# Kernel tuning notes

Hardware: AMD Instinct MI355X
Metric: run time of the kernel (lower is better)

The kernel has to match this reference:

```python
import jax, jax.numpy as jnp
import numpy as np

N = 50000   # nodes
E = 800000  # edges
NF = 16     # num_node_features
EF = 8      # num_edge_features
H = 4       # heads
C = 64      # out_channels per head
NC = 4      # num_classes


def setup_inputs() -> dict:
    key = jax.random.key(0)
    ks = jax.random.split(key, 32)
    w = lambda k, shape: (jax.random.normal(k, shape, jnp.float32) * 0.05)
    inp = {
        "x": jax.random.normal(ks[0], (N, NF), jnp.float32),
        "edge_index": jax.random.randint(ks[1], (2, E), 0, N, dtype=jnp.int32),
        "edge_attr": jax.random.normal(ks[2], (E, EF), jnp.float32),
        # fc00
        "w00": w(ks[3], (NF, 64)), "b00": jnp.zeros((64,), jnp.float32),
        # edge MLP
        "we1": w(ks[4], (EF, 64)), "be1": jnp.zeros((64,), jnp.float32),
        "we2": w(ks[5], (64, 64)), "be2": jnp.zeros((64,), jnp.float32),
        "we3": w(ks[6], (64, 64)), "be3": jnp.zeros((64,), jnp.float32),
        # TransformerConv projections (64 -> H*C = 256)
        "wq": w(ks[7], (64, H * C)), "bq": jnp.zeros((H * C,), jnp.float32),
        "wk": w(ks[8], (64, H * C)), "bk": jnp.zeros((H * C,), jnp.float32),
        "wv": w(ks[9], (64, H * C)), "bv": jnp.zeros((H * C,), jnp.float32),
        "wedge": w(ks[10], (64, H * C)), "bedge": jnp.zeros((H * C,), jnp.float32),
        "wskip": w(ks[11], (64, H * C)), "bskip": jnp.zeros((H * C,), jnp.float32),
        # LayerNorm(256)
        "ln_g": jnp.ones((H * C,), jnp.float32), "ln_b": jnp.zeros((H * C,), jnp.float32),
        # head
        "w1": w(ks[12], (H * C, 128)), "b1": jnp.zeros((128,), jnp.float32),
        "w2": w(ks[13], (128, NC)), "b2": jnp.zeros((NC,), jnp.float32),
    }
    return inp


def _forward(x, edge_attr, w00, b00, we1, be1, we2, be2, we3, be3,
             wq, bq, wk, bk, wv, bv, wedge, bedge, wskip, bskip,
             ln_g, ln_b, w1, b1, w2, b2, edge_index):
    relu = jax.nn.relu
    n = x.shape[0]
    # node embed (dropout = identity in eval)
    x1 = relu(x @ w00 + b00)                              # [N, 64]
    # edge MLP
    e = relu(edge_attr @ we1 + be1)
    e = relu(e @ we2 + be2)
    e = relu(e @ we3 + be3)                               # [E, 64]
    src, dst = edge_index[0], edge_index[1]
    # project nodes once, then gather per edge
    q = (x1 @ wq + bq).reshape(n, H, C)[dst]              # [E, H, C]
    k = (x1 @ wk + bk).reshape(n, H, C)[src]
    v = (x1 @ wv + bv).reshape(n, H, C)[src]
    eh = (e @ wedge + bedge).reshape(-1, H, C)            # [E, H, C]
    k = k + eh
    v = v + eh
    alpha = jnp.sum(q * k, axis=-1) / np.sqrt(C)          # [E, H]
    # segment softmax over incoming edges of each target node
    m = jax.ops.segment_max(alpha, dst, num_segments=n)   # [N, H]
    m = jnp.where(jnp.isfinite(m), m, 0.0)
    p = jnp.exp(alpha - m[dst])
    s = jax.ops.segment_sum(p, dst, num_segments=n)
    a = p / (s[dst] + 1e-16)                              # [E, H]
    out = jax.ops.segment_sum(v * a[:, :, None], dst, num_segments=n)
    out = out.reshape(n, H * C) + (x1 @ wskip + bskip)    # root skip (root_weight=True)
    # LayerNorm(256)
    mu = jnp.mean(out, axis=-1, keepdims=True)
    var = jnp.mean(jnp.square(out - mu), axis=-1, keepdims=True)
    out = (out - mu) * jax.lax.rsqrt(var + 1e-5) * ln_g + ln_b
    out = relu(out)
    h = relu(out @ w1 + b1)
    logits = h @ w2 + b2
    return jax.nn.log_softmax(logits, axis=1)


def reference(x, edge_index, edge_attr, w00, b00, we1, be1, we2, be2, we3, be3,
              wq, bq, wk, bk, wv, bv, wedge, bedge, wskip, bskip,
              ln_g, ln_b, w1, b1, w2, b2):
    return _forward(x, edge_attr, w00, b00, we1, be1, we2, be2, we3, be3,
                    wq, bq, wk, bk, wv, bv, wedge, bedge, wskip, bskip,
                    ln_g, ln_b, w1, b1, w2, b2, edge_index)
```

## Files before the change

### kernel.cpp

```cpp
#include <hip/hip_runtime.h>
#include <hip/hip_bf16.h>

typedef unsigned short u16;
typedef __attribute__((ext_vector_type(8))) short bf16x8;
typedef __attribute__((ext_vector_type(4))) float f32x4;

#define NN 50000
#define NE 800000
#define SCAN_NB ((NN + 255) / 256)

__device__ __forceinline__ float bf2f(u16 u) { return __uint_as_float(((unsigned)u) << 16); }
__device__ __forceinline__ u16 f2bf(float f) {
  unsigned u = __float_as_uint(f);
  return (u16)((u + 0x7FFFu + ((u >> 16) & 1u)) >> 16);
}

__global__ void k_zero(int* __restrict__ deg) {
  int i = blockIdx.x * 256 + threadIdx.x;
  if (i < NN) deg[i] = 0;
}

__global__ void k_hist(const int* __restrict__ ei, int* __restrict__ deg) {
  int i = blockIdx.x * 256 + threadIdx.x;
  if (i < NE) {
    int d = ei[NE + i];
    if (d >= 0 && d < NN) atomicAdd(&deg[d], 1);
  }
}

__global__ __launch_bounds__(256) void k_scan_a(const int* __restrict__ deg,
                                                int* __restrict__ bsum) {
  __shared__ int red[256];
  const int t = threadIdx.x;
  const int i = blockIdx.x * 256 + t;
  red[t] = (i < NN) ? deg[i] : 0;
  __syncthreads();
  #pragma unroll
  for (int s = 128; s > 0; s >>= 1) {
    if (t < s) red[t] += red[t + s];
    __syncthreads();
  }
  if (t == 0) bsum[blockIdx.x] = red[0];
}

__global__ __launch_bounds__(256) void k_scan_b(const int* __restrict__ bsum,
                                                int* __restrict__ boff,
                                                int* __restrict__ rowptr) {
  __shared__ int s[256];
  const int t = threadIdx.x;
  int v = (t < SCAN_NB) ? bsum[t] : 0;
  s[t] = v;
  __syncthreads();
  #pragma unroll
  for (int o = 1; o < 256; o <<= 1) {
    int u = (t >= o) ? s[t - o] : 0;
    __syncthreads();
    s[t] += u;
    __syncthreads();
  }
  if (t < SCAN_NB) boff[t] = s[t] - v;
  if (t == 255) rowptr[NN] = s[255];
}

__global__ __launch_bounds__(256) void k_scan_c(const int* __restrict__ deg,
                                                const int* __restrict__ boff,
                                                int* __restrict__ rowptr,
                                                int* __restrict__ cursor) {
  __shared__ int s[256];
  const int t = threadIdx.x;
  const int i = blockIdx.x * 256 + t;
  int v = (i < NN) ? deg[i] : 0;
  s[t] = v;
  __syncthreads();
  #pragma unroll
  for (int o = 1; o < 256; o <<= 1) {
    int u = (t >= o) ? s[t - o] : 0;
    __syncthreads();
    s[t] += u;
    __syncthreads();
  }
  if (i < NN) {
    int r = boff[blockIdx.x] + s[t] - v;
    rowptr[i] = r;
    cursor[i] = r;
  }
}

__global__ void k_scatter(const int* __restrict__ ei, int* __restrict__ cursor,
                          int* __restrict__ slist, int* __restrict__ e2p) {
  int i = blockIdx.x * 256 + threadIdx.x;
  if (i < NE) {
    int d = ei[NE + i];
    if (d >= 0 && d < NN) {
      int pos = atomicAdd(&cursor[d], 1);
      if (pos >= 0 && pos < NE) {
        e2p[i] = pos;
        int s = ei[i];
        slist[pos] = max(0, min(s, NN - 1));
      }
    }
  }
}

__global__ void k_prep(const float* __restrict__ wedge, const float* __restrict__ wk,
                       float* __restrict__ wT, float* __restrict__ wkT) {
  int i = blockIdx.x * 256 + threadIdx.x;
  if (i < 16384) {
    int c = i >> 6, j = i & 63;
    wT[i] = wedge[j * 256 + c];
  } else if (i < 32768) {
    int i2 = i - 16384;
    int c = i2 >> 6, j = i2 & 63;
    wkT[i2] = wk[j * 256 + c];
  }
}

__global__ void k_prep_w(const float* __restrict__ we1, const float* __restrict__ we2,
                         const float* __restrict__ we3,
                         u16* __restrict__ wB1t, u16* __restrict__ wB2t, u16* __restrict__ wB3t) {
  int i = blockIdx.x * 256 + threadIdx.x;
  if (i < 512) {
    int n = i >> 3, k = i & 7;
    wB1t[i] = f2bf(we1[k * 64 + n]);
  } else if (i < 512 + 4096) {
    int i2 = i - 512;
    int n = i2 >> 6, k = i2 & 63;
    wB2t[i2] = f2bf(we2[k * 64 + n]);
  } else if (i < 512 + 8192) {
    int i2 = i - 512 - 4096;
    int n = i2 >> 6, k = i2 & 63;
    wB3t[i2] = f2bf(we3[k * 64 + n]);
  }
}

__global__ void k_prep_b(const float* __restrict__ wedge, const float* __restrict__ wv,
                         const float* __restrict__ wskip, u16* __restrict__ Bt) {
  const int col = blockIdx.x;
  const int k = threadIdx.x;
  float v;
  if (k < 256) v = ((k >> 6) == (col >> 6)) ? wedge[(k & 63) * 256 + col] : 0.f;
  else if (k < 512) { int k2 = k - 256; v = ((k2 >> 6) == (col >> 6)) ? wv[(k2 & 63) * 256 + col] : 0.f; }
  else v = wskip[(k - 512) * 256 + col];
  Bt[col * 576 + k] = f2bf(v);
}

__global__ void k_prep_h(const float* __restrict__ w1, u16* __restrict__ Bt1) {
  const int col = blockIdx.x;
  const int k = threadIdx.x;
  Bt1[col * 256 + k] = f2bf(w1[k * 128 + col]);
}

__global__ __launch_bounds__(256) void k_ng(
    const float* __restrict__ x, const float* __restrict__ w00, const float* __restrict__ b00,
    const float* __restrict__ wq, const float* __restrict__ bq,
    const float* __restrict__ wT, const float* __restrict__ wkT,
    u16* __restrict__ x1g, u16* __restrict__ Gg, u16* __restrict__ Qkg) {
  __shared__ float xs[128];
  __shared__ float x1s[8 * 65];
  __shared__ float qs[8 * 256];
  const int t = threadIdx.x;
  const int n0 = blockIdx.x * 8;
  if (t < 128) xs[t] = x[n0 * 16 + t];
  __syncthreads();
  #pragma unroll
  for (int it = 0; it < 2; ++it) {
    int nb = it * 4 + (t >> 6);
    int col = t & 63;
    float v = b00[col];
    #pragma unroll
    for (int i = 0; i < 16; ++i) v += xs[nb * 16 + i] * w00[i * 64 + col];
    v = fmaxf(v, 0.f);
    x1s[nb * 65 + col] = v;
    x1g[(n0 + nb) * 64 + col] = f2bf(v);
  }
  __syncthreads();
  {
    float aq[8];
    const float bqv = bq[t];
    #pragma unroll
    for (int nb = 0; nb < 8; ++nb) aq[nb] = bqv;
    for (int j = 0; j < 64; ++j) {
      float wqv = wq[j * 256 + t];
      #pragma unroll
      for (int nb = 0; nb < 8; ++nb) aq[nb] += x1s[nb * 65 + j] * wqv;
    }
    #pragma unroll
    for (int nb = 0; nb < 8; ++nb) qs[nb * 256 + t] = aq[nb];
  }
  __syncthreads();
  const int h = t >> 6, j = t & 63;
  float accG[8] = {0, 0, 0, 0, 0, 0, 0, 0};
  float accK[8] = {0, 0, 0, 0, 0, 0, 0, 0};
  for (int c = 0; c < 64; ++c) {
    float wv = wT[(h * 64 + c) * 64 + j];
    float wk = wkT[(h * 64 + c) * 64 + j];
    #pragma unroll
    for (int nb = 0; nb < 8; ++nb) {
      float qv = qs[nb * 256 + h * 64 + c];
      accG[nb] += qv * wv;
      accK[nb] += qv * wk;
    }
  }
  #pragma unroll
  for (int nb = 0; nb < 8; ++nb) {
    Gg[(n0 + nb) * 256 + t] = f2bf(accG[nb]);
    Qkg[(n0 + nb) * 256 + t] = f2bf(accK[nb]);
  }
}

#define EPB 128
#define APAD 72
__global__ __launch_bounds__(256) void k_edge_mlp(
    const float* __restrict__ ea,
    const u16* __restrict__ wB1t, const u16* __restrict__ wB2t, const u16* __restrict__ wB3t,
    const float* __restrict__ be1, const float* __restrict__ be2, const float* __restrict__ be3,
    const int* __restrict__ e2p, u16* __restrict__ e3g) {
  __shared__ u16 actA[EPB * APAD];
  __shared__ u16 actB[EPB * APAD];
  const int t = threadIdx.x;
  const int w = t >> 6, l = t & 63;
  const int quad = l >> 4, li = l & 15;
  const int e0 = blockIdx.x * EPB;
  const f32x4 zc = {0.f, 0.f, 0.f, 0.f};

  float b1c[4], b2c[4], b3c[4];
  #pragma unroll
  for (int nt = 0; nt < 4; ++nt) {
    b1c[nt] = be1[nt * 16 + li];
    b2c[nt] = be2[nt * 16 + li];
    b3c[nt] = be3[nt * 16 + li];
  }

  bf16x8 b1f[4];
  #pragma unroll
  for (int nt = 0; nt < 4; ++nt) {
    bf16x8 z = {};
    if (quad == 0) z = *(const bf16x8*)(wB1t + (nt * 16 + li) * 8);
    b1f[nt] = z;
  }
  #pragma unroll
  for (int mi = 0; mi < 2; ++mi) {
    const int mt = w * 2 + mi;
    bf16x8 af = {};
    if (quad == 0) {
      const float4* pa = (const float4*)(ea + (size_t)(e0 + mt * 16 + li) * 8);
      float4 p0 = pa[0], p1 = pa[1];
      af[0] = (short)f2bf(p0.x); af[1] = (short)f2bf(p0.y);
      af[2] = (short)f2bf(p0.z); af[3] = (short)f2bf(p0.w);
      af[4] = (short)f2bf(p1.x); af[5] = (short)f2bf(p1.y);
      af[6] = (short)f2bf(p1.z); af[7] = (short)f2bf(p1.w);
    }
    #pragma unroll
    for (int nt = 0; nt < 4; ++nt) {
      f32x4 d = __builtin_amdgcn_mfma_f32_16x16x32_bf16(af, b1f[nt], zc, 0, 0, 0);
      #pragma unroll
      for (int r = 0; r < 4; ++r)
        actA[(mt * 16 + quad * 4 + r) * APAD + nt * 16 + li] = f2bf(fmaxf(d[r] + b1c[nt], 0.f));
    }
  }
  __syncthreads();

  {
    bf16x8 bf[4][2];
    #pragma unroll
    for (int nt = 0; nt < 4; ++nt)
      #pragma unroll
      for (int kk = 0; kk < 2; ++kk)
        bf[nt][kk] = *(const bf16x8*)(wB2t + (nt * 16 + li) * 64 + kk * 32 + quad * 8);
    #pragma unroll
    for (int mi = 0; mi < 2; ++mi) {
      const int mt = w * 2 + mi;
      bf16x8 a0 = *(const bf16x8*)(actA + (mt * 16 + li) * APAD + quad * 8);
      bf16x8 a1 = *(const bf16x8*)(actA + (mt * 16 + li) * APAD + 32 + quad * 8);
      #pragma unroll
      for (int nt = 0; nt < 4; ++nt) {
        f32x4 d = __builtin_amdgcn_mfma_f32_16x16x32_bf16(a0, bf[nt][0], zc, 0, 0, 0);
        d = __builtin_amdgcn_mfma_f32_16x16x32_bf16(a1, bf[nt][1], d, 0, 0, 0);
        #pragma unroll
        for (int r = 0; r < 4; ++r)
          actB[(mt * 16 + quad * 4 + r) * APAD + nt * 16 + li] = f2bf(fmaxf(d[r] + b2c[nt], 0.f));
      }
    }
  }
  __syncthreads();

  {
    bf16x8 bf[4][2];
    #pragma unroll
    for (int nt = 0; nt < 4; ++nt)
      #pragma unroll
      for (int kk = 0; kk < 2; ++kk)
        bf[nt][kk] = *(const bf16x8*)(wB3t + (nt * 16 + li) * 64 + kk * 32 + quad * 8);
    #pragma unroll
    for (int mi = 0; mi < 2; ++mi) {
      const int mt = w * 2 + mi;
      bf16x8 a0 = *(const bf16x8*)(actB + (mt * 16 + li) * APAD + quad * 8);
      bf16x8 a1 = *(const bf16x8*)(actB + (mt * 16 + li) * APAD + 32 + quad * 8);
      #pragma unroll
      for (int nt = 0; nt < 4; ++nt) {
        f32x4 d = __builtin_amdgcn_mfma_f32_16x16x32_bf16(a0, bf[nt][0], zc, 0, 0, 0);
        d = __builtin_amdgcn_mfma_f32_16x16x32_bf16(a1, bf[nt][1], d, 0, 0, 0);
        #pragma unroll
        for (int r = 0; r < 4; ++r)
          actA[(mt * 16 + quad * 4 + r) * APAD + nt * 16 + li] = f2bf(fmaxf(d[r] + b3c[nt], 0.f));
      }
    }
  }
  __syncthreads();

  #pragma unroll
  for (int it = 0; it < 4; ++it) {
    int flat = it * 2048 + t * 8;
    int el = flat >> 6, c = flat & 63;
    int pos = e2p[e0 + el];
    pos = ((unsigned)pos <= (unsigned)(NE - 1)) ? pos : NE;
    uint4 v = *(const uint4*)(actA + el * APAD + c);
    *(uint4*)(e3g + (size_t)pos * 64 + c) = v;
  }
}

__global__ __launch_bounds__(256) void k_attn(
    const int* __restrict__ rowptr, const int* __restrict__ slist,
    u16* yo, const u16* __restrict__ x1g, u16* gz, const u16* __restrict__ Qkg,
    const u16* __restrict__ e3g, float* __restrict__ bfac) {
  const int t = threadIdx.x;
  const int w = t >> 6;
  const int l = t & 63;
  const int grp = l >> 4;
  const int li = l & 15;
  const int chb = grp * 64 + li * 4;
  const int n = blockIdx.x * 4 + w;
  int base = rowptr[n];
  int end  = rowptr[n + 1];
  base = max(0, min(base, NE));
  end  = max(base, min(end, NE));
  if (l == 0) bfac[n] = (end > base) ? 1.f : 0.f;

  float Qkf[4], Gf[4];
  {
    ushort4 kv = *(const ushort4*)(Qkg + (size_t)n * 256 + chb);
    Qkf[0] = bf2f(kv.x); Qkf[1] = bf2f(kv.y); Qkf[2] = bf2f(kv.z); Qkf[3] = bf2f(kv.w);
    ushort4 gv = *(const ushort4*)(gz + (size_t)n * 256 + chb);
    Gf[0] = bf2f(gv.x); Gf[1] = bf2f(gv.y); Gf[2] = bf2f(gv.z); Gf[3] = bf2f(gv.w);
  }

  float s_run = 0.f;
  float y[4] = {0, 0, 0, 0}, zz[4] = {0, 0, 0, 0};
  int d = base;
  for (; d + 1 < end; d += 2) {
    int src0 = slist[d], src1 = slist[d + 1];
    src0 = max(0, min(src0, NN - 1)); src1 = max(0, min(src1, NN - 1));
    ushort4 x0 = *(const ushort4*)(x1g + (size_t)src0 * 64 + li * 4);
    ushort4 e0 = *(const ushort4*)(e3g + (size_t)d * 64 + li * 4);
    ushort4 x1v = *(const ushort4*)(x1g + (size_t)src1 * 64 + li * 4);
    ushort4 e1 = *(const ushort4*)(e3g + (size_t)(d + 1) * 64 + li * 4);
    float xf00 = bf2f(x0.x), xf01 = bf2f(x0.y), xf02 = bf2f(x0.z), xf03 = bf2f(x0.w);
    float ef00 = bf2f(e0.x), ef01 = bf2f(e0.y), ef02 = bf2f(e0.z), ef03 = bf2f(e0.w);
    float xf10 = bf2f(x1v.x), xf11 = bf2f(x1v.y), xf12 = bf2f(x1v.z), xf13 = bf2f(x1v.w);
    float ef10 = bf2f(e1.x), ef11 = bf2f(e1.y), ef12 = bf2f(e1.z), ef13 = bf2f(e1.w);
    float p0 = Qkf[0]*xf00 + Qkf[1]*xf01 + Qkf[2]*xf02 + Qkf[3]*xf03
             + Gf[0]*ef00 + Gf[1]*ef01 + Gf[2]*ef02 + Gf[3]*ef03;
    float p1 = Qkf[0]*xf10 + Qkf[1]*xf11 + Qkf[2]*xf12 + Qkf[3]*xf13
             + Gf[0]*ef10 + Gf[1]*ef11 + Gf[2]*ef12 + Gf[3]*ef13;
    #pragma unroll
    for (int mk = 1; mk < 16; mk <<= 1) { p0 += __shfl_xor(p0, mk); p1 += __shfl_xor(p1, mk); }
    float w0 = __expf(fminf(p0 * 0.125f, 60.f));
    float w1 = __expf(fminf(p1 * 0.125f, 60.f));
    s_run += w0 + w1;
    y[0] += w0*xf00 + w1*xf10; y[1] += w0*xf01 + w1*xf11;
    y[2] += w0*xf02 + w1*xf12; y[3] += w0*xf03 + w1*xf13;
    zz[0] += w0*ef00 + w1*ef10; zz[1] += w0*ef01 + w1*ef11;
    zz[2] += w0*ef02 + w1*ef12; zz[3] += w0*ef03 + w1*ef13;
  }
  if (d < end) {
    int src0 = slist[d];
    src0 = max(0, min(src0, NN - 1));
    ushort4 x0 = *(const ushort4*)(x1g + (size_t)src0 * 64 + li * 4);
    ushort4 e0 = *(const ushort4*)(e3g + (size_t)d * 64 + li * 4);
    float xf00 = bf2f(x0.x), xf01 = bf2f(x0.y), xf02 = bf2f(x0.z), xf03 = bf2f(x0.w);
    float ef00 = bf2f(e0.x), ef01 = bf2f(e0.y), ef02 = bf2f(e0.z), ef03 = bf2f(e0.w);
    float p0 = Qkf[0]*xf00 + Qkf[1]*xf01 + Qkf[2]*xf02 + Qkf[3]*xf03
             + Gf[0]*ef00 + Gf[1]*ef01 + Gf[2]*ef02 + Gf[3]*ef03;
    #pragma unroll
    for (int mk = 1; mk < 16; mk <<= 1) p0 += __shfl_xor(p0, mk);
    float w0 = __expf(fminf(p0 * 0.125f, 60.f));
    s_run += w0;
    y[0] += w0*xf00; y[1] += w0*xf01; y[2] += w0*xf02; y[3] += w0*xf03;
    zz[0] += w0*ef00; zz[1] += w0*ef01; zz[2] += w0*ef02; zz[3] += w0*ef03;
  }
  const float inv_s = 1.0f / (s_run + 1e-16f);
  ushort4 ynv, znv;
  ynv.x = f2bf(y[0] * inv_s); ynv.y = f2bf(y[1] * inv_s);
  ynv.z = f2bf(y[2] * inv_s); ynv.w = f2bf(y[3] * inv_s);
  znv.x = f2bf(zz[0] * inv_s); znv.y = f2bf(zz[1] * inv_s);
  znv.z = f2bf(zz[2] * inv_s); znv.w = f2bf(zz[3] * inv_s);
  *(ushort4*)(yo + (size_t)n * 256 + chb) = ynv;
  *(ushort4*)(gz + (size_t)n * 256 + chb) = znv;
}

#define PM 64
#define PK 576
#define PAPAD 584
__global__ __launch_bounds__(256) void k_post(
    const u16* __restrict__ zng, const u16* __restrict__ yng, const u16* __restrict__ x1g,
    const u16* __restrict__ Bt, const float* __restrict__ bfac,
    const float* __restrict__ bedge, const float* __restrict__ bv, const float* __restrict__ bskip,
    const float* __restrict__ lng, const float* __restrict__ lnb,
    u16* __restrict__ postg) {
  __shared__ u16 As[PM * PAPAD];
  __shared__ float ps1[PM * 4];
  __shared__ float ps2[PM * 4];
  const int t = threadIdx.x;
  const int w = t >> 6, l = t & 63;
  const int quad = l >> 4, li = l & 15;
  const int n0 = blockIdx.x * PM;

  for (int q = t; q < 2048; q += 256) {
    int row = q >> 5, off = (q & 31) * 8;
    uint4 vz = make_uint4(0, 0, 0, 0), vy = make_uint4(0, 0, 0, 0);
    if (n0 + row < NN) {
      vz = *(const uint4*)(zng + (size_t)(n0 + row) * 256 + off);
      vy = *(const uint4*)(yng + (size_t)(n0 + row) * 256 + off);
    }
    *(uint4*)(As + row * PAPAD + off) = vz;
    *(uint4*)(As + row * PAPAD + 256 + off) = vy;
  }
  for (int q = t; q < 512; q += 256) {
    int row = q >> 3, off = (q & 7) * 8;
    uint4 v = make_uint4(0, 0, 0, 0);
    if (n0 + row < NN) v = *(const uint4*)(x1g + (size_t)(n0 + row) * 64 + off);
    *(uint4*)(As + row * PAPAD + 512 + off) = v;
  }
  __syncthreads();

  f32x4 acc[4][4];
  #pragma unroll
  for (int mt = 0; mt < 4; ++mt)
    #pragma unroll
    for (int nt = 0; nt < 4; ++nt) acc[mt][nt] = (f32x4){0.f, 0.f, 0.f, 0.f};

  const int colbase = w * 64;
  #pragma unroll
  for (int s = 0; s < 18; ++s) {
    bf16x8 bf[4];
    #pragma unroll
    for (int nt = 0; nt < 4; ++nt)
      bf[nt] = *(const bf16x8*)(Bt + (size_t)(colbase + nt * 16 + li) * PK + s * 32 + quad * 8);
    #pragma unroll
    for (int mt = 0; mt < 4; ++mt) {
      bf16x8 af = *(const bf16x8*)(As + (mt * 16 + li) * PAPAD + s * 32 + quad * 8);
      #pragma unroll
      for (int nt = 0; nt < 4; ++nt)
        acc[mt][nt] = __builtin_amdgcn_mfma_f32_16x16x32_bf16(af, bf[nt], acc[mt][nt], 0, 0, 0);
    }
  }

  float beb[4], bs4[4], g4[4], lb4[4];
  #pragma unroll
  for (int nt = 0; nt < 4; ++nt) {
    int col = colbase + nt * 16 + li;
    beb[nt] = bedge[col] + bv[col];
    bs4[nt] = bskip[col]; g4[nt] = lng[col]; lb4[nt] = lnb[col];
  }
  #pragma unroll
  for (int mt = 0; mt < 4; ++mt) {
    #pragma unroll
    for (int r = 0; r < 4; ++r) {
      int node = n0 + mt * 16 + quad * 4 + r;
      float hasE = bfac[min(node, NN - 1)];
      #pragma unroll
      for (int nt = 0; nt < 4; ++nt)
        acc[mt][nt][r] += hasE * beb[nt] + bs4[nt];
    }
  }
  #pragma unroll
  for (int mt = 0; mt < 4; ++mt)
    #pragma unroll
    for (int r = 0; r < 4; ++r) {
      float s = acc[mt][0][r] + acc[mt][1][r] + acc[mt][2][r] + acc[mt][3][r];
      #pragma unroll
      for (int mk = 1; mk < 16; mk <<= 1) s += __shfl_xor(s, mk);
      if (li == 0) ps1[(mt * 16 + quad * 4 + r) * 4 + w] = s;
    }
  __syncthreads();
  float mu[4][4];
  #pragma unroll
  for (int mt = 0; mt < 4; ++mt)
    #pragma unroll
    for (int r = 0; r < 4; ++r) {
      float4 p = *(const float4*)(ps1 + (mt * 16 + quad * 4 + r) * 4);
      mu[mt][r] = (p.x + p.y + p.z + p.w) * (1.0f / 256.0f);
    }
  #pragma unroll
  for (int mt = 0; mt < 4; ++mt)
    #pragma unroll
    for (int r = 0; r < 4; ++r) {
      float m = mu[mt][r];
      float s = 0.f;
      #pragma unroll
      for (int nt = 0; nt < 4; ++nt) { float dd = acc[mt][nt][r] - m; s += dd * dd; }
      #pragma unroll
      for (int mk = 1; mk < 16; mk <<= 1) s += __shfl_xor(s, mk);
      if (li == 0) ps2[(mt * 16 + quad * 4 + r) * 4 + w] = s;
    }
  __syncthreads();
  #pragma unroll
  for (int mt = 0; mt < 4; ++mt)
    #pragma unroll
    for (int r = 0; r < 4; ++r) {
      float4 p = *(const float4*)(ps2 + (mt * 16 + quad * 4 + r) * 4);
      float rstd = rsqrtf((p.x + p.y + p.z + p.w) * (1.0f / 256.0f) + 1e-5f);
      int node = n0 + mt * 16 + quad * 4 + r;
      if (node < NN) {
        float m = mu[mt][r];
        #pragma unroll
        for (int nt = 0; nt < 4; ++nt) {
          int col = colbase + nt * 16 + li;
          postg[(size_t)node * 256 + col] =
              f2bf(fmaxf((acc[mt][nt][r] - m) * rstd * g4[nt] + lb4[nt], 0.f));
        }
      }
    }
}

#define HAPAD 264
#define H1PAD 136
__global__ __launch_bounds__(256) void k_head(
    const u16* __restrict__ postg, const u16* __restrict__ Bt1,
    const float* __restrict__ b1, const float* __restrict__ w2, const float* __restrict__ b2,
    float* __restrict__ outg) {
  __shared__ u16 As[64 * HAPAD];
  __shared__ u16 h1s[64 * H1PAD];
  const int t = threadIdx.x;
  const int w = t >> 6, l = t & 63;
  const int quad = l >> 4, li = l & 15;
  const int n0 = blockIdx.x * 64;

  for (int q = t; q < 2048; q += 256) {
    int row = q >> 5, off = (q & 31) * 8;
    uint4 v = make_uint4(0, 0, 0, 0);
    if (n0 + row < NN) v = *(const uint4*)(postg + (size_t)(n0 + row) * 256 + off);
    *(uint4*)(As + row * HAPAD + off) = v;
  }
  __syncthreads();

  f32x4 acc[4][2];
  #pragma unroll
  for (int mt = 0; mt < 4; ++mt)
    #pragma unroll
    for (int nt = 0; nt < 2; ++nt) acc[mt][nt] = (f32x4){0.f, 0.f, 0.f, 0.f};
  const int colbase = w * 32;
  #pragma unroll
  for (int s = 0; s < 8; ++s) {
    bf16x8 bf[2];
    #pragma unroll
    for (int nt = 0; nt < 2; ++nt)
      bf[nt] = *(const bf16x8*)(Bt1 + (size_t)(colbase + nt * 16 + li) * 256 + s * 32 + quad * 8);
    #pragma unroll
    for (int mt = 0; mt < 4; ++mt) {
      bf16x8 af = *(const bf16x8*)(As + (mt * 16 + li) * HAPAD + s * 32 + quad * 8);
      #pragma unroll
      for (int nt = 0; nt < 2; ++nt)
        acc[mt][nt] = __builtin_amdgcn_mfma_f32_16x16x32_bf16(af, bf[nt], acc[mt][nt], 0, 0, 0);
    }
  }
  float b1c[2];
  #pragma unroll
  for (int nt = 0; nt < 2; ++nt) b1c[nt] = b1[colbase + nt * 16 + li];
  #pragma unroll
  for (int mt = 0; mt < 4; ++mt)
    #pragma unroll
    for (int nt = 0; nt < 2; ++nt)
      #pragma unroll
      for (int r = 0; r < 4; ++r)
        h1s[(mt * 16 + quad * 4 + r) * H1PAD + colbase + nt * 16 + li] =
            f2bf(fmaxf(acc[mt][nt][r] + b1c[nt], 0.f));
  __syncthreads();

  const int node = t >> 2, c = t & 3;
  float lg = b2[c];
  const u16* hrow = h1s + node * H1PAD;
  #pragma unroll 4
  for (int j = 0; j < 128; ++j) lg += bf2f(hrow[j]) * w2[j * 4 + c];
  float mx = lg;
  #pragma unroll
  for (int mk = 1; mk < 4; mk <<= 1) mx = fmaxf(mx, __shfl_xor(mx, mk));
  float ex = __expf(lg - mx);
  float se = ex;
  #pragma unroll
  for (int mk = 1; mk < 4; mk <<= 1) se += __shfl_xor(se, mk);
  float res = lg - (mx + __logf(se));
  if (n0 + node < NN) outg[(size_t)(n0 + node) * 4 + c] = res;
}

extern "C" void kernel_launch(void* const* d_in, const int* in_sizes, int n_in,
                              void* d_out, int out_size, void* d_ws, size_t ws_size,
                              hipStream_t stream) {
  const float* x     = (const float*)d_in[0];
  const int*   ei    = (const int*)d_in[1];
  const float* ea    = (const float*)d_in[2];
  const float* w00   = (const float*)d_in[3];
  const float* b00   = (const float*)d_in[4];
  const float* we1   = (const float*)d_in[5];
  const float* be1   = (const float*)d_in[6];
  const float* we2   = (const float*)d_in[7];
  const float* be2   = (const float*)d_in[8];
  const float* we3   = (const float*)d_in[9];
  const float* be3   = (const float*)d_in[10];
  const float* wq    = (const float*)d_in[11];
  const float* bq    = (const float*)d_in[12];
  const float* wk    = (const float*)d_in[13];
  const float* bk    = (const float*)d_in[14];
  const float* wv    = (const float*)d_in[15];
  const float* bv    = (const float*)d_in[16];
  const float* wedge = (const float*)d_in[17];
  const float* bedge = (const float*)d_in[18];
  const float* wskip = (const float*)d_in[19];
  const float* bskip = (const float*)d_in[20];
  const float* lng   = (const float*)d_in[21];
  const float* lnb   = (const float*)d_in[22];
  const float* w1    = (const float*)d_in[23];
  const float* b1    = (const float*)d_in[24];
  const float* w2    = (const float*)d_in[25];
  const float* b2    = (const float*)d_in[26];
  float* outg = (float*)d_out;
  (void)bk;

  size_t off = 0;
  char* wsb = (char*)d_ws;
  auto carve = [&](size_t bytes) -> char* {
    char* r = wsb + off;
    off += (bytes + 255) & ~(size_t)255;
    return r;
  };
  u16* yg     = (u16*)carve((size_t)NN * 256 * 2);
  u16* Gg     = (u16*)carve((size_t)NN * 256 * 2);
  u16* Qkg    = (u16*)carve((size_t)NN * 256 * 2);
  u16* x1g    = (u16*)carve((size_t)NN * 64 * 2);
  u16* e3g    = (u16*)carve((size_t)(NE + 1) * 64 * 2);
  int* deg    = (int*)carve((size_t)NN * 4);
  int* rowptr = (int*)carve((size_t)(NN + 1) * 4);
  int* cursor = (int*)carve((size_t)NN * 4);
  int* slist  = (int*)carve((size_t)NE * 4);
  int* e2p    = (int*)carve((size_t)NE * 4);
  float* bfac = (float*)carve((size_t)NN * 4);
  int* bsum   = (int*)carve((size_t)SCAN_NB * 4);
  int* boff   = (int*)carve((size_t)SCAN_NB * 4);
  float* wT   = (float*)carve(16384 * 4);
  float* wkT  = (float*)carve(16384 * 4);
  u16* wB1t   = (u16*)carve(512 * 2);
  u16* wB2t   = (u16*)carve(4096 * 2);
  u16* wB3t   = (u16*)carve(4096 * 2);
  u16* Bt     = (u16*)carve((size_t)256 * 576 * 2);
  u16* Bt1    = (u16*)carve((size_t)128 * 256 * 2);
  u16* postg  = e3g;
  if (off > ws_size) return;

  k_prep<<<128, 256, 0, stream>>>(wedge, wk, wT, wkT);
  k_prep_w<<<34, 256, 0, stream>>>(we1, we2, we3, wB1t, wB2t, wB3t);
  k_prep_b<<<256, 576, 0, stream>>>(wedge, wv, wskip, Bt);
  k_prep_h<<<128, 256, 0, stream>>>(w1, Bt1);
  k_zero<<<SCAN_NB, 256, 0, stream>>>(deg);
  k_hist<<<NE / 256, 256, 0, stream>>>(ei, deg);
  k_scan_a<<<SCAN_NB, 256, 0, stream>>>(deg, bsum);
  k_scan_b<<<1, 256, 0, stream>>>(bsum, boff, rowptr);
  k_scan_c<<<SCAN_NB, 256, 0, stream>>>(deg, boff, rowptr, cursor);
  k_scatter<<<NE / 256, 256, 0, stream>>>(ei, cursor, slist, e2p);
  k_ng<<<NN / 8, 256, 0, stream>>>(x, w00, b00, wq, bq, wT, wkT, x1g, Gg, Qkg);
  k_edge_mlp<<<NE / EPB, 256, 0, stream>>>(ea, wB1t, wB2t, wB3t, be1, be2, be3, e2p, e3g);
  k_attn<<<NN / 4, 256, 0, stream>>>(rowptr, slist, yg, x1g, Gg, Qkg, e3g, bfac);
  k_post<<<(NN + PM - 1) / PM, 256, 0, stream>>>(Gg, yg, x1g, Bt, bfac, bedge, bv, bskip,
                                                 lng, lnb, postg);
  k_head<<<(NN + 63) / 64, 256, 0, stream>>>(postg, Bt1, b1, w2, b2, outg);
}
```

Before: 550.8 us.

## Rewrite node projection kernel with bf16 MFMA over 64-node tiles

The node-projection kernel moves from scalar fp32 FMAs on 8 nodes per block to bf16 MFMA matrix instructions on 64 nodes per block. It covers the x->x1 embedding, the Q projection, and the per-head G and Qk projections, which now use block-diagonal packed weights. A new prep kernel transposes and converts those weights to bf16. The aim is to cut the ALU cost of the node-side GEMMs and reuse weights across more nodes, at the price of bf16 rounding of q before the second projection and extra zero work in the block-diagonal matrix.

```diff
diff --git a/kernel.cpp b/kernel.cpp
--- a/kernel.cpp
+++ b/kernel.cpp
@@ -102,16 +102,24 @@
   }
 }
 
-__global__ void k_prep(const float* __restrict__ wedge, const float* __restrict__ wk,
-                       float* __restrict__ wT, float* __restrict__ wkT) {
+__global__ void k_prep_ng(const float* __restrict__ w00, const float* __restrict__ wq,
+                          const float* __restrict__ wedge, const float* __restrict__ wk,
+                          u16* __restrict__ wB00t, u16* __restrict__ wqt, u16* __restrict__ BGQ) {
   int i = blockIdx.x * 256 + threadIdx.x;
-  if (i < 16384) {
-    int c = i >> 6, j = i & 63;
-    wT[i] = wedge[j * 256 + c];
-  } else if (i < 32768) {
-    int i2 = i - 16384;
-    int c = i2 >> 6, j = i2 & 63;
-    wkT[i2] = wk[j * 256 + c];
+  if (i < 2048) {
+    int n = i >> 5, k = i & 31;
+    wB00t[i] = (k < 16) ? f2bf(w00[k * 64 + n]) : (u16)0;
+  } else if (i < 2048 + 16384) {
+    int i2 = i - 2048;
+    int n = i2 >> 6, k = i2 & 63;
+    wqt[i2] = f2bf(wq[k * 256 + n]);
+  } else if (i < 2048 + 16384 + 131072) {
+    int i2 = i - 2048 - 16384;
+    int col = i2 >> 8, k = i2 & 255;
+    float v;
+    if (col < 256) v = ((k >> 6) == (col >> 6)) ? wedge[(col & 63) * 256 + k] : 0.f;
+    else { int c = col - 256; v = ((k >> 6) == (c >> 6)) ? wk[(c & 63) * 256 + k] : 0.f; }
+    BGQ[i2] = f2bf(v);
   }
 }
 
@@ -151,60 +159,117 @@
 }
 
 __global__ __launch_bounds__(256) void k_ng(
-    const float* __restrict__ x, const float* __restrict__ w00, const float* __restrict__ b00,
-    const float* __restrict__ wq, const float* __restrict__ bq,
-    const float* __restrict__ wT, const float* __restrict__ wkT,
+    const float* __restrict__ x, const u16* __restrict__ wB00t, const float* __restrict__ b00,
+    const u16* __restrict__ wqt, const float* __restrict__ bq,
+    const u16* __restrict__ BGQ,
     u16* __restrict__ x1g, u16* __restrict__ Gg, u16* __restrict__ Qkg) {
-  __shared__ float xs[128];
-  __shared__ float x1s[8 * 65];
-  __shared__ float qs[8 * 256];
+  __shared__ u16 xs[64 * 32];
+  __shared__ u16 x1s[64 * 72];
+  __shared__ u16 qs[64 * 264];
   const int t = threadIdx.x;
-  const int n0 = blockIdx.x * 8;
-  if (t < 128) xs[t] = x[n0 * 16 + t];
-  __syncthreads();
+  const int w = t >> 6, l = t & 63;
+  const int quad = l >> 4, li = l & 15;
+  const int n0 = blockIdx.x * 64;
+  const f32x4 zc = {0.f, 0.f, 0.f, 0.f};
+
+  for (int q = t; q < 2048; q += 256) {
+    int row = q >> 5, k = q & 31;
+    float v = (k < 16 && n0 + row < NN) ? x[(size_t)(n0 + row) * 16 + k] : 0.f;
+    xs[row * 32 + k] = f2bf(v);
+  }
+  __syncthreads();
+
+  {
+    bf16x8 bf = *(const bf16x8*)(wB00t + (w * 16 + li) * 32 + quad * 8);
+    float bc = b00[w * 16 + li];
+    #pragma unroll
+    for (int mt = 0; mt < 4; ++mt) {
+      bf16x8 af = *(const bf16x8*)(xs + (mt * 16 + li) * 32 + quad * 8);
+      f32x4 d = __builtin_amdgcn_mfma_f32_16x16x32_bf16(af, bf, zc, 0, 0, 0);
+      #pragma unroll
+      for (int r = 0; r < 4; ++r)
+        x1s[(mt * 16 + quad * 4 + r) * 72 + w * 16 + li] = f2bf(fmaxf(d[r] + bc, 0.f));
+    }
+  }
+  __syncthreads();
+
   #pragma unroll
   for (int it = 0; it < 2; ++it) {
-    int nb = it * 4 + (t >> 6);
-    int col = t & 63;
-    float v = b00[col];
-    #pragma unroll
-    for (int i = 0; i < 16; ++i) v += xs[nb * 16 + i] * w00[i * 64 + col];
-    v = fmaxf(v, 0.f);
-    x1s[nb * 65 + col] = v;
-    x1g[(n0 + nb) * 64 + col] = f2bf(v);
-  }
-  __syncthreads();
+    int i = (it * 256 + t) * 8;
+    int row = i >> 6, col = i & 63;
+    if (n0 + row < NN)
+      *(uint4*)(x1g + (size_t)(n0 + row) * 64 + col) = *(const uint4*)(x1s + row * 72 + col);
+  }
+
   {
-    float aq[8];
-    const float bqv = bq[t];
-    #pragma unroll
-    for (int nb = 0; nb < 8; ++nb) aq[nb] = bqv;
-    for (int j = 0; j < 64; ++j) {
-      float wqv = wq[j * 256 + t];
-      #pragma unroll
-      for (int nb = 0; nb < 8; ++nb) aq[nb] += x1s[nb * 65 + j] * wqv;
-    }
-    #pragma unroll
-    for (int nb = 0; nb < 8; ++nb) qs[nb * 256 + t] = aq[nb];
-  }
-  __syncthreads();
-  const int h = t >> 6, j = t & 63;
-  float accG[8] = {0, 0, 0, 0, 0, 0, 0, 0};
-  float accK[8] = {0, 0, 0, 0, 0, 0, 0, 0};
-  for (int c = 0; c < 64; ++c) {
-    float wv = wT[(h * 64 + c) * 64 + j];
-    float wk = wkT[(h * 64 + c) * 64 + j];
-    #pragma unroll
-    for (int nb = 0; nb < 8; ++nb) {
-      float qv = qs[nb * 256 + h * 64 + c];
-      accG[nb] += qv * wv;
-      accK[nb] += qv * wk;
-    }
-  }
-  #pragma unroll
-  for (int nb = 0; nb < 8; ++nb) {
-    Gg[(n0 + nb) * 256 + t] = f2bf(accG[nb]);
-    Qkg[(n0 + nb) * 256 + t] = f2bf(accK[nb]);
+    f32x4 acc[4][4];
+    #pragma unroll
+    for (int mt = 0; mt < 4; ++mt)
+      #pragma unroll
+      for (int nt = 0; nt < 4; ++nt) acc[mt][nt] = zc;
+    const int colbase = w * 64;
+    #pragma unroll
+    for (int s = 0; s < 2; ++s) {
+      bf16x8 bf[4];
+      #pragma unroll
+      for (int nt = 0; nt < 4; ++nt)
+        bf[nt] = *(const bf16x8*)(wqt + (size_t)(colbase + nt * 16 + li) * 64 + s * 32 + quad * 8);
+      #pragma unroll
+      for (int mt = 0; mt < 4; ++mt) {
+        bf16x8 af = *(const bf16x8*)(x1s + (mt * 16 + li) * 72 + s * 32 + quad * 8);
+        #pragma unroll
+        for (int nt = 0; nt < 4; ++nt)
+          acc[mt][nt] = __builtin_amdgcn_mfma_f32_16x16x32_bf16(af, bf[nt], acc[mt][nt], 0, 0, 0);
+      }
+    }
+    float bqc[4];
+    #pragma unroll
+    for (int nt = 0; nt < 4; ++nt) bqc[nt] = bq[colbase + nt * 16 + li];
+    #pragma unroll
+    for (int mt = 0; mt < 4; ++mt)
+      #pragma unroll
+      for (int nt = 0; nt < 4; ++nt)
+        #pragma unroll
+        for (int r = 0; r < 4; ++r)
+          qs[(mt * 16 + quad * 4 + r) * 264 + colbase + nt * 16 + li] = f2bf(acc[mt][nt][r] + bqc[nt]);
+  }
+  __syncthreads();
+
+  #pragma unroll
+  for (int half = 0; half < 2; ++half) {
+    f32x4 acc[4][4];
+    #pragma unroll
+    for (int mt = 0; mt < 4; ++mt)
+      #pragma unroll
+      for (int nt = 0; nt < 4; ++nt) acc[mt][nt] = zc;
+    const int colbase = w * 64;
+    const size_t bofs = (size_t)(half * 256) * 256;
+    #pragma unroll
+    for (int s = 0; s < 8; ++s) {
+      bf16x8 bf[4];
+      #pragma unroll
+      for (int nt = 0; nt < 4; ++nt)
+        bf[nt] = *(const bf16x8*)(BGQ + bofs + (size_t)(colbase + nt * 16 + li) * 256 + s * 32 + quad * 8);
+      #pragma unroll
+      for (int mt = 0; mt < 4; ++mt) {
+        bf16x8 af = *(const bf16x8*)(qs + (mt * 16 + li) * 264 + s * 32 + quad * 8);
+        #pragma unroll
+        for (int nt = 0; nt < 4; ++nt)
+          acc[mt][nt] = __builtin_amdgcn_mfma_f32_16x16x32_bf16(af, bf[nt], acc[mt][nt], 0, 0, 0);
+      }
+    }
+    u16* dst = half ? Qkg : Gg;
+    #pragma unroll
+    for (int mt = 0; mt < 4; ++mt)
+      #pragma unroll
+      for (int r = 0; r < 4; ++r) {
+        int node = n0 + mt * 16 + quad * 4 + r;
+        if (node < NN) {
+          #pragma unroll
+          for (int nt = 0; nt < 4; ++nt)
+            dst[(size_t)node * 256 + colbase + nt * 16 + li] = f2bf(acc[mt][nt][r]);
+        }
+      }
   }
 }
 
@@ -646,8 +711,9 @@
   float* bfac = (float*)carve((size_t)NN * 4);
   int* bsum   = (int*)carve((size_t)SCAN_NB * 4);
   int* boff   = (int*)carve((size_t)SCAN_NB * 4);
-  float* wT   = (float*)carve(16384 * 4);
-  float* wkT  = (float*)carve(16384 * 4);
+  u16* wB00t  = (u16*)carve(2048 * 2);
+  u16* wqt    = (u16*)carve(16384 * 2);
+  u16* BGQ    = (u16*)carve((size_t)131072 * 2);
   u16* wB1t   = (u16*)carve(512 * 2);
   u16* wB2t   = (u16*)carve(4096 * 2);
   u16* wB3t   = (u16*)carve(4096 * 2);
@@ -656,7 +722,7 @@
   u16* postg  = e3g;
   if (off > ws_size) return;
 
-  k_prep<<<128, 256, 0, stream>>>(wedge, wk, wT, wkT);
+  k_prep_ng<<<584, 256, 0, stream>>>(w00, wq, wedge, wk, wB00t, wqt, BGQ);
   k_prep_w<<<34, 256, 0, stream>>>(we1, we2, we3, wB1t, wB2t, wB3t);
   k_prep_b<<<256, 576, 0, stream>>>(wedge, wv, wskip, Bt);
   k_prep_h<<<128, 256, 0, stream>>>(w1, Bt1);
@@ -666,7 +732,7 @@
   k_scan_b<<<1, 256, 0, stream>>>(bsum, boff, rowptr);
   k_scan_c<<<SCAN_NB, 256, 0, stream>>>(deg, boff, rowptr, cursor);
   k_scatter<<<NE / 256, 256, 0, stream>>>(ei, cursor, slist, e2p);
-  k_ng<<<NN / 8, 256, 0, stream>>>(x, w00, b00, wq, bq, wT, wkT, x1g, Gg, Qkg);
+  k_ng<<<(NN + 63) / 64, 256, 0, stream>>>(x, wB00t, b00, wqt, bq, BGQ, x1g, Gg, Qkg);
   k_edge_mlp<<<NE / EPB, 256, 0, stream>>>(ea, wB1t, wB2t, wB3t, be1, be2, be3, e2p, e3g);
   k_attn<<<NN / 4, 256, 0, stream>>>(rowptr, slist, yg, x1g, Gg, Qkg, e3g, bfac);
   k_post<<<(NN + PM - 1) / PM, 256, 0, stream>>>(Gg, yg, x1g, Bt, bfac, bedge, bv, bskip,
```

After: 499.0 us. 1.1x faster.
